# Performance work log

Hardware: AMD Instinct MI355X
Metric: run time of the kernel (lower is better)

## Reference

```python
import jax, jax.numpy as jnp
import numpy as np

B, S, IN_DIM = 8, 1024, 512
EMBED_DIM, NUM_HEADS = 512, 8
HEAD_DIM = EMBED_DIM // NUM_HEADS
LN_EPS = 1e-5


def setup_inputs() -> dict:
    key = jax.random.key(0)
    k1, k2, k3 = jax.random.split(key, 3)
    x = jax.random.normal(k1, (B, S, IN_DIM), dtype=jnp.float32)
    # xavier_uniform for qkv_proj.weight [3*embed, in] and o_proj.weight [embed, embed]
    lim_qkv = float(np.sqrt(6.0 / (3 * EMBED_DIM + IN_DIM)))
    w_qkv = jax.random.uniform(k2, (3 * EMBED_DIM, IN_DIM), dtype=jnp.float32,
                               minval=-lim_qkv, maxval=lim_qkv)
    lim_o = float(np.sqrt(6.0 / (EMBED_DIM + EMBED_DIM)))
    w_o = jax.random.uniform(k3, (EMBED_DIM, EMBED_DIM), dtype=jnp.float32,
                             minval=-lim_o, maxval=lim_o)
    return {"x": x, "w_qkv": w_qkv, "w_o": w_o}


def reference(x, w_qkv, w_o):
    b, s, _ = x.shape
    # fused QKV projection: [b, s, 3*embed]
    qkv = jnp.einsum('bsi,ei->bse', x, w_qkv)
    # [b, h, s, 3*head_dim]
    qkv = qkv.reshape(b, s, NUM_HEADS, 3 * HEAD_DIM).transpose(0, 2, 1, 3)
    q, k, v = jnp.split(qkv, 3, axis=-1)
    scale = 1.0 / np.sqrt(HEAD_DIM)
    logits = jnp.einsum('bhqd,bhkd->bhqk', q, k) * scale  # [b, h, s, s]
    attn = jax.nn.softmax(logits, axis=-1)
    vals = jnp.einsum('bhqk,bhkd->bhqd', attn, v)
    vals = vals.transpose(0, 2, 1, 3).reshape(b, s, EMBED_DIM)
    o = jnp.einsum('bse,fe->bsf', vals, w_o)
    # LayerNorm over [seq, embed] jointly (fresh nn.LayerNorm([N, D]): weight=1, bias=0)
    mu = jnp.mean(o, axis=(-2, -1), keepdims=True)
    var = jnp.var(o, axis=(-2, -1), keepdims=True)
    o = (o - mu) / jnp.sqrt(var + LN_EPS)
    return o
```

## Files before the change

### kernel.cpp

```cpp
#include <hip/hip_runtime.h>
#include <hip/hip_bf16.h>
#include <math.h>

#define BB 8
#define SS 1024
#define INDIM 512
#define ED 512
#define NH 8
#define HD 64

typedef __attribute__((ext_vector_type(8))) short short8;
typedef __attribute__((ext_vector_type(4))) float f32x4;
typedef __attribute__((ext_vector_type(16))) float f32x16;
typedef unsigned short u16;

typedef __attribute__((address_space(1))) const void gv_t;
typedef __attribute__((address_space(3))) void lv_t;

static __device__ __forceinline__ u16 f2bf(float f) {
  union { float f; unsigned u; } v; v.f = f;
  unsigned r = v.u + 0x7fffu + ((v.u >> 16) & 1u);
  return (u16)(r >> 16);
}
static __device__ __forceinline__ float bf2f(u16 b) {
  union { unsigned u; float f; } v; v.u = (unsigned)b << 16; return v.f;
}

static __device__ __forceinline__ unsigned cvt_pk_bf16(float a, float b) {
  unsigned r;
  asm("v_cvt_pk_bf16_f32 %0, %1, %2" : "=v"(r) : "v"(a), "v"(b));
  return r;
}
static __device__ __forceinline__ float fast_exp2(float x) {
  float r; asm("v_exp_f32 %0, %1" : "=v"(r) : "v"(x)); return r;
}

__global__ void cvt_all(const float* __restrict__ x, const float* __restrict__ wq,
                        const float* __restrict__ wo, u16* __restrict__ xb,
                        u16* __restrict__ wqb, u16* __restrict__ wob) {
  const int n1 = 1048576;
  const int n2 = n1 + 196608;
  const int n3 = n2 + 65536;
  int i = blockIdx.x * blockDim.x + threadIdx.x;
  int stride = gridDim.x * blockDim.x;
  for (; i < n3; i += stride) {
    const float4* src; ushort4* dst; int j;
    if (i < n1)      { src = (const float4*)x;  dst = (ushort4*)xb;  j = i; }
    else if (i < n2) { src = (const float4*)wq; dst = (ushort4*)wqb; j = i - n1; }
    else             { src = (const float4*)wo; dst = (ushort4*)wob; j = i - n2; }
    float4 v = src[j];
    ushort4 o;
    o.x = f2bf(v.x); o.y = f2bf(v.y); o.z = f2bf(v.z); o.w = f2bf(v.w);
    dst[j] = o;
  }
}

template<int EPI>
__global__ __launch_bounds__(256, 2)
void gemm_nt(const u16* __restrict__ A, const u16* __restrict__ Bm, int K,
             u16* __restrict__ outB,
             u16* __restrict__ qws, u16* __restrict__ kws, u16* __restrict__ vtws,
             float2* __restrict__ partials)
{
  __shared__ u16 As[128][64];
  __shared__ u16 Bs[128][64];
  const int tid = threadIdx.x;
  const int lane = tid & 63;
  const int wv = tid >> 6;
  const int wr = wv >> 1, wc = wv & 1;
  const int bm = blockIdx.x, bn = blockIdx.y;
  const int l15 = lane & 15, lg = lane >> 4;
  const int srow8 = lane >> 3;
  const int sc8 = lane & 7;

  f32x4 acc[4][4];
  #pragma unroll
  for (int i = 0; i < 4; i++)
    #pragma unroll
    for (int j = 0; j < 4; j++) acc[i][j] = (f32x4){0.f, 0.f, 0.f, 0.f};

  for (int kk = 0; kk < K; kk += 64) {
    #pragma unroll
    for (int i = 0; i < 4; i++) {
      int r0 = (i * 4 + wv) * 8;
      int r = r0 + srow8;
      int cs = sc8 ^ (r & 7);
      const u16* ga = A + (size_t)(bm * 128 + r) * K + kk + cs * 8;
      __builtin_amdgcn_global_load_lds((gv_t*)ga, (lv_t*)&As[r0][0], 16, 0, 0);
      const u16* gb = Bm + (size_t)(bn * 128 + r) * K + kk + cs * 8;
      __builtin_amdgcn_global_load_lds((gv_t*)gb, (lv_t*)&Bs[r0][0], 16, 0, 0);
    }
    __syncthreads();
    #pragma unroll
    for (int kc = 0; kc < 2; kc++) {
      short8 af[4], bf[4];
      #pragma unroll
      for (int mi = 0; mi < 4; mi++) {
        int ra = wr * 64 + mi * 16 + l15;
        af[mi] = *(const short8*)&As[ra][((kc * 4 + lg) ^ (ra & 7)) * 8];
      }
      #pragma unroll
      for (int ni = 0; ni < 4; ni++) {
        int rb = wc * 64 + ni * 16 + l15;
        bf[ni] = *(const short8*)&Bs[rb][((kc * 4 + lg) ^ (rb & 7)) * 8];
      }
      #pragma unroll
      for (int mi = 0; mi < 4; mi++)
        #pragma unroll
        for (int ni = 0; ni < 4; ni++)
          acc[mi][ni] = __builtin_amdgcn_mfma_f32_16x16x32_bf16(af[mi], bf[ni], acc[mi][ni], 0, 0, 0);
    }
    __syncthreads();
  }

  if constexpr (EPI == 0) {
    #pragma unroll
    for (int mi = 0; mi < 4; mi++) {
      int rowg = bm * 128 + wr * 64 + mi * 16 + lg * 4;
      #pragma unroll
      for (int ni = 0; ni < 4; ni++) {
        int colg = bn * 128 + wc * 64 + ni * 16 + l15;
        int h = colg / 192, c = colg - h * 192;
        #pragma unroll
        for (int r = 0; r < 4; r++) {
          int rg = rowg + r;
          float v = acc[mi][ni][r];
          int b = rg >> 10, s = rg & 1023;
          int bh = b * 8 + h;
          if (c < 64)
            qws[((size_t)(bh * 1024 + s)) * 64 + c] = f2bf(v * 0.18033688f);
          else if (c < 128)
            kws[((size_t)(bh * 1024 + s)) * 64 + (c - 64)] = f2bf(v);
        }
      }
    }
    const int rem = (bn * 128) % 192;
    if (rem != 0) {
      __shared__ u16 T[64][136];
      const int vbase = (rem == 128) ? 0 : 64;
      if (wc == (vbase >> 6)) {
        #pragma unroll
        for (int mi = 0; mi < 4; mi++) {
          int trow0 = wr * 64 + mi * 16 + lg * 4;
          #pragma unroll
          for (int ni = 0; ni < 4; ni++) {
            int tcol = ni * 16 + l15;
            u16 tmp[4];
            #pragma unroll
            for (int r = 0; r < 4; r++) tmp[r] = f2bf(acc[mi][ni][r]);
            *(uint2*)&T[tcol][trow0] = *(const uint2*)tmp;
          }
        }
      }
      __syncthreads();
      const int h = (bn * 128 + vbase) / 192;
      const int bh = (bm >> 3) * 8 + h;
      const int col = tid >> 2, q4 = tid & 3;
      u16* dst = vtws + ((size_t)(bh * 64 + col)) * 1024 + (bm & 7) * 128 + q4 * 32;
      const u16* src = &T[col][q4 * 32];
      #pragma unroll
      for (int k2 = 0; k2 < 4; k2++)
        *(uint4*)(dst + k2 * 8) = *(const uint4*)(src + k2 * 8);
    }
  } else {
    float s1 = 0.f, s2 = 0.f;
    #pragma unroll
    for (int mi = 0; mi < 4; mi++) {
      int rowg = bm * 128 + wr * 64 + mi * 16 + lg * 4;
      #pragma unroll
      for (int ni = 0; ni < 4; ni++) {
        int colg = bn * 128 + wc * 64 + ni * 16 + l15;
        #pragma unroll
        for (int r = 0; r < 4; r++) {
          float v = acc[mi][ni][r];
          s1 += v; s2 += v * v;
          outB[(size_t)(rowg + r) * 512 + colg] = f2bf(v);
        }
      }
    }
    #pragma unroll
    for (int off = 1; off < 64; off <<= 1) {
      s1 += __shfl_xor(s1, off);
      s2 += __shfl_xor(s2, off);
    }
    __shared__ float r1[4], r2[4];
    if (lane == 0) { r1[wv] = s1; r2[wv] = s2; }
    __syncthreads();
    if (tid == 0) {
      float t1 = r1[0] + r1[1] + r1[2] + r1[3];
      float t2 = r2[0] + r2[1] + r2[2] + r2[3];
      partials[bm * 4 + bn] = make_float2(t1, t2);
    }
  }
}

__global__ __launch_bounds__(512, 4)
void attn_kernel(const u16* __restrict__ qws, const u16* __restrict__ kws,
                 const u16* __restrict__ vtws, u16* __restrict__ vals)
{
  __shared__ __align__(16) u16 Ksm[2][64][72];
  __shared__ __align__(16) u16 Vsm[2][64][72];
  const int tid = threadIdx.x;
  const int lane = tid & 63;
  const int wq = tid >> 6;
  const int l31 = lane & 31;
  const int hi = lane >> 5;
  const int logical = (blockIdx.x & 7) * 32 + (blockIdx.x >> 3);
  const int bh = logical >> 2;
  const int q0 = (logical & 3) * 256;

  short8 qf[4];
  {
    const u16* qp = qws + ((size_t)bh * 1024 + q0 + wq * 32 + l31) * 64 + 8 * hi;
    #pragma unroll
    for (int j = 0; j < 4; j++) qf[j] = *(const short8*)(qp + 16 * j);
  }

  const int srow = tid >> 3;
  const int sc8 = (tid & 7) * 8;
  uint4 kreg, vreg;
  kreg = *(const uint4*)(kws + ((size_t)bh * 1024 + srow) * 64 + sc8);
  vreg = *(const uint4*)(vtws + ((size_t)(bh * 64 + srow)) * 1024 + sc8);
  *(uint4*)&Ksm[0][srow][sc8] = kreg;
  *(uint4*)&Vsm[0][srow][sc8] = vreg;
  __syncthreads();

  f32x16 o[2];
  #pragma unroll
  for (int r = 0; r < 16; r++) { o[0][r] = 0.f; o[1][r] = 0.f; }
  float m = -1e30f, l = 0.f;

  for (int t = 0; t < 16; t++) {
    const int cur = t & 1;
    if (t < 15) {
      int kv = (t + 1) * 64;
      kreg = *(const uint4*)(kws + ((size_t)bh * 1024 + kv + srow) * 64 + sc8);
      vreg = *(const uint4*)(vtws + ((size_t)(bh * 64 + srow)) * 1024 + kv + sc8);
    }

    f32x16 stv[2];
    __builtin_amdgcn_s_setprio(1);
    #pragma unroll
    for (int s2 = 0; s2 < 2; s2++) {
      f32x16 c;
      #pragma unroll
      for (int r = 0; r < 16; r++) c[r] = 0.f;
      #pragma unroll
      for (int j = 0; j < 4; j++) {
        short8 kf = *(const short8*)&Ksm[cur][s2 * 32 + l31][16 * j + 8 * hi];
        c = __builtin_amdgcn_mfma_f32_32x32x16_bf16(kf, qf[j], c, 0, 0, 0);
      }
      stv[s2] = c;
    }
    __builtin_amdgcn_s_setprio(0);

    float mx[16];
    #pragma unroll
    for (int r = 0; r < 16; r++) mx[r] = fmaxf(stv[0][r], stv[1][r]);
    #pragma unroll
    for (int w = 8; w >= 1; w >>= 1)
      #pragma unroll
      for (int r = 0; r < w; r++) mx[r] = fmaxf(mx[r], mx[r + w]);
    float pm = fmaxf(mx[0], __shfl_xor(mx[0], 32));

    if (!__all(pm - m <= 10.0f)) {
      float mn = fmaxf(m, pm);
      float al = fast_exp2(m - mn);
      m = mn; l *= al;
      #pragma unroll
      for (int reg = 0; reg < 16; reg++) {
        int qrow = (reg & 3) + 8 * (reg >> 2) + 4 * hi;
        float alo = __shfl(al, qrow);
        o[0][reg] *= alo; o[1][reg] *= alo;
      }
    }

    unsigned pk[16];
    float ps[16];
    #pragma unroll
    for (int s2 = 0; s2 < 2; s2++)
      #pragma unroll
      for (int j = 0; j < 8; j++) {
        float p0 = fast_exp2(stv[s2][2 * j] - m);
        float p1 = fast_exp2(stv[s2][2 * j + 1] - m);
        ps[s2 * 8 + j] = p0 + p1;
        pk[s2 * 8 + j] = cvt_pk_bf16(p0, p1);
      }
    #pragma unroll
    for (int w = 8; w >= 1; w >>= 1)
      #pragma unroll
      for (int r = 0; r < w; r++) ps[r] += ps[r + w];
    l += ps[0] + __shfl_xor(ps[0], 32);

    short8 pa[4];
    #pragma unroll
    for (int cc = 0; cc < 4; cc++) {
      int base = (cc >> 1) * 8 + (cc & 1) * 4;
      unsigned a0 = pk[base + 0], a2 = pk[base + 2];
      unsigned a1 = pk[base + 1], a3 = pk[base + 3];
      asm volatile("v_permlane32_swap_b32 %0, %1" : "+v"(a0), "+v"(a2));
      asm volatile("v_permlane32_swap_b32 %0, %1" : "+v"(a1), "+v"(a3));
      union { unsigned u[4]; short8 s8; } uu;
      uu.u[0] = a0; uu.u[1] = a1; uu.u[2] = a2; uu.u[3] = a3;
      pa[cc] = uu.s8;
    }

    __builtin_amdgcn_s_setprio(1);
    #pragma unroll
    for (int dh = 0; dh < 2; dh++)
      #pragma unroll
      for (int cc = 0; cc < 4; cc++) {
        short8 vf = *(const short8*)&Vsm[cur][dh * 32 + l31][16 * cc + 8 * hi];
        o[dh] = __builtin_amdgcn_mfma_f32_32x32x16_bf16(pa[cc], vf, o[dh], 0, 0, 0);
      }
    __builtin_amdgcn_s_setprio(0);

    if (t < 15) {
      *(uint4*)&Ksm[cur ^ 1][srow][sc8] = kreg;
      *(uint4*)&Vsm[cur ^ 1][srow][sc8] = vreg;
    }
    __syncthreads();
  }

  const int b = bh >> 3, h = bh & 7;
  #pragma unroll
  for (int reg = 0; reg < 16; reg++) {
    int qrow = (reg & 3) + 8 * (reg >> 2) + 4 * hi;
    float linv = 1.0f / __shfl(l, qrow);
    size_t grow = (size_t)(b * 1024 + q0 + wq * 32 + qrow) * 512 + h * 64;
    vals[grow + l31]      = f2bf(o[0][reg] * linv);
    vals[grow + 32 + l31] = f2bf(o[1][reg] * linv);
  }
}

__global__ void ln_norm3(const u16* __restrict__ ob, float* __restrict__ o,
                         const float2* __restrict__ partials) {
  const int blk = blockIdx.x;
  const int b = blk >> 8;
  const int lane = threadIdx.x & 63;
  float s1 = 0.f, s2 = 0.f;
  if (lane < 32) {
    float2 p = partials[b * 32 + lane];
    s1 = p.x; s2 = p.y;
  }
  #pragma unroll
  for (int off = 1; off < 64; off <<= 1) {
    s1 += __shfl_xor(s1, off);
    s2 += __shfl_xor(s2, off);
  }
  float mu = s1 / 524288.f;
  float rs = rsqrtf(s2 / 524288.f - mu * mu + 1e-5f);
  const size_t i = (size_t)blk * 2048 + threadIdx.x * 8;
  uint4 v = *(const uint4*)(ob + i);
  float4 o0, o1;
  o0.x = (bf2f((u16)(v.x & 0xffff)) - mu) * rs;
  o0.y = (bf2f((u16)(v.x >> 16)) - mu) * rs;
  o0.z = (bf2f((u16)(v.y & 0xffff)) - mu) * rs;
  o0.w = (bf2f((u16)(v.y >> 16)) - mu) * rs;
  o1.x = (bf2f((u16)(v.z & 0xffff)) - mu) * rs;
  o1.y = (bf2f((u16)(v.z >> 16)) - mu) * rs;
  o1.z = (bf2f((u16)(v.w & 0xffff)) - mu) * rs;
  o1.w = (bf2f((u16)(v.w >> 16)) - mu) * rs;
  *(float4*)(o + i) = o0;
  *(float4*)(o + i + 4) = o1;
}

extern "C" void kernel_launch(void* const* d_in, const int* in_sizes, int n_in,
                              void* d_out, int out_size, void* d_ws, size_t ws_size,
                              hipStream_t stream) {
  const float* x = (const float*)d_in[0];
  const float* wqkv = (const float*)d_in[1];
  const float* wo = (const float*)d_in[2];
  float* out = (float*)d_out;
  char* ws = (char*)d_ws;

  u16* xb        = (u16*)(ws + 0);
  u16* wqb       = (u16*)(ws + 8388608);
  u16* wob       = (u16*)(ws + 9961472);
  u16* qws       = (u16*)(ws + 10485760);
  u16* kws       = (u16*)(ws + 18874368);
  u16* vtws      = (u16*)(ws + 27262976);
  u16* vals      = (u16*)(ws + 35651584);
  u16* outb      = (u16*)(ws + 44040192);
  float2* parts  = (float2*)(ws + 52428800);

  cvt_all<<<1280, 256, 0, stream>>>(x, wqkv, wo, xb, wqb, wob);

  dim3 g1(64, 12);
  gemm_nt<0><<<g1, 256, 0, stream>>>(xb, wqb, 512, nullptr, qws, kws, vtws, nullptr);

  attn_kernel<<<256, 512, 0, stream>>>(qws, kws, vtws, vals);

  dim3 g2(64, 4);
  gemm_nt<1><<<g2, 256, 0, stream>>>(vals, wob, 512, outb, nullptr, nullptr, nullptr, parts);

  ln_norm3<<<2048, 256, 0, stream>>>(outb, out, parts);
}
```

Before: 76.37 us.

## Fuse output projection GEMM with LayerNorm via cooperative grid sync

Merges the output-projection GEMM and the LayerNorm normalisation into one cooperative kernel. Each block computes its partial sums, all blocks meet at a grid-wide sync, and each block then normalises its accumulators still in registers and writes fp32 output directly. This removes the bf16 intermediate write and read and one kernel launch. In exchange it adds the cost of a grid barrier and a cooperative launch, and it requires all 256 blocks to be resident at the same time.

```diff
diff --git a/kernel.cpp b/kernel.cpp
--- a/kernel.cpp
+++ b/kernel.cpp
@@ -1,6 +1,9 @@
 #include <hip/hip_runtime.h>
 #include <hip/hip_bf16.h>
+#include <hip/hip_cooperative_groups.h>
 #include <math.h>
+
+namespace cg = cooperative_groups;
 
 #define BB 8
 #define SS 1024
@@ -55,12 +58,9 @@
   }
 }
 
-template<int EPI>
 __global__ __launch_bounds__(256, 2)
-void gemm_nt(const u16* __restrict__ A, const u16* __restrict__ Bm, int K,
-             u16* __restrict__ outB,
-             u16* __restrict__ qws, u16* __restrict__ kws, u16* __restrict__ vtws,
-             float2* __restrict__ partials)
+void gemm_qkv(const u16* __restrict__ A, const u16* __restrict__ Bm, int K,
+              u16* __restrict__ qws, u16* __restrict__ kws, u16* __restrict__ vtws)
 {
   __shared__ u16 As[128][64];
   __shared__ u16 Bs[128][64];
@@ -113,83 +113,161 @@
     __syncthreads();
   }
 
-  if constexpr (EPI == 0) {
-    #pragma unroll
-    for (int mi = 0; mi < 4; mi++) {
-      int rowg = bm * 128 + wr * 64 + mi * 16 + lg * 4;
+  #pragma unroll
+  for (int mi = 0; mi < 4; mi++) {
+    int rowg = bm * 128 + wr * 64 + mi * 16 + lg * 4;
+    #pragma unroll
+    for (int ni = 0; ni < 4; ni++) {
+      int colg = bn * 128 + wc * 64 + ni * 16 + l15;
+      int h = colg / 192, c = colg - h * 192;
+      #pragma unroll
+      for (int r = 0; r < 4; r++) {
+        int rg = rowg + r;
+        float v = acc[mi][ni][r];
+        int b = rg >> 10, s = rg & 1023;
+        int bh = b * 8 + h;
+        if (c < 64)
+          qws[((size_t)(bh * 1024 + s)) * 64 + c] = f2bf(v * 0.18033688f);
+        else if (c < 128)
+          kws[((size_t)(bh * 1024 + s)) * 64 + (c - 64)] = f2bf(v);
+      }
+    }
+  }
+  const int rem = (bn * 128) % 192;
+  if (rem != 0) {
+    __shared__ u16 T[64][136];
+    const int vbase = (rem == 128) ? 0 : 64;
+    if (wc == (vbase >> 6)) {
+      #pragma unroll
+      for (int mi = 0; mi < 4; mi++) {
+        int trow0 = wr * 64 + mi * 16 + lg * 4;
+        #pragma unroll
+        for (int ni = 0; ni < 4; ni++) {
+          int tcol = ni * 16 + l15;
+          u16 tmp[4];
+          #pragma unroll
+          for (int r = 0; r < 4; r++) tmp[r] = f2bf(acc[mi][ni][r]);
+          *(uint2*)&T[tcol][trow0] = *(const uint2*)tmp;
+        }
+      }
+    }
+    __syncthreads();
+    const int h = (bn * 128 + vbase) / 192;
+    const int bh = (bm >> 3) * 8 + h;
+    const int col = tid >> 2, q4 = tid & 3;
+    u16* dst = vtws + ((size_t)(bh * 64 + col)) * 1024 + (bm & 7) * 128 + q4 * 32;
+    const u16* src = &T[col][q4 * 32];
+    #pragma unroll
+    for (int k2 = 0; k2 < 4; k2++)
+      *(uint4*)(dst + k2 * 8) = *(const uint4*)(src + k2 * 8);
+  }
+}
+
+__global__ __launch_bounds__(256, 2)
+void gemm_o_ln(const u16* __restrict__ A, const u16* __restrict__ Bm,
+               float* __restrict__ outF, float2* __restrict__ partials)
+{
+  __shared__ u16 As[128][64];
+  __shared__ u16 Bs[128][64];
+  const int K = 512;
+  const int tid = threadIdx.x;
+  const int lane = tid & 63;
+  const int wv = tid >> 6;
+  const int wr = wv >> 1, wc = wv & 1;
+  const int bm = blockIdx.x, bn = blockIdx.y;
+  const int l15 = lane & 15, lg = lane >> 4;
+  const int srow8 = lane >> 3;
+  const int sc8 = lane & 7;
+
+  f32x4 acc[4][4];
+  #pragma unroll
+  for (int i = 0; i < 4; i++)
+    #pragma unroll
+    for (int j = 0; j < 4; j++) acc[i][j] = (f32x4){0.f, 0.f, 0.f, 0.f};
+
+  for (int kk = 0; kk < K; kk += 64) {
+    #pragma unroll
+    for (int i = 0; i < 4; i++) {
+      int r0 = (i * 4 + wv) * 8;
+      int r = r0 + srow8;
+      int cs = sc8 ^ (r & 7);
+      const u16* ga = A + (size_t)(bm * 128 + r) * K + kk + cs * 8;
+      __builtin_amdgcn_global_load_lds((gv_t*)ga, (lv_t*)&As[r0][0], 16, 0, 0);
+      const u16* gb = Bm + (size_t)(bn * 128 + r) * K + kk + cs * 8;
+      __builtin_amdgcn_global_load_lds((gv_t*)gb, (lv_t*)&Bs[r0][0], 16, 0, 0);
+    }
+    __syncthreads();
+    #pragma unroll
+    for (int kc = 0; kc < 2; kc++) {
+      short8 af[4], bf[4];
+      #pragma unroll
+      for (int mi = 0; mi < 4; mi++) {
+        int ra = wr * 64 + mi * 16 + l15;
+        af[mi] = *(const short8*)&As[ra][((kc * 4 + lg) ^ (ra & 7)) * 8];
+      }
       #pragma unroll
       for (int ni = 0; ni < 4; ni++) {
-        int colg = bn * 128 + wc * 64 + ni * 16 + l15;
-        int h = colg / 192, c = colg - h * 192;
+        int rb = wc * 64 + ni * 16 + l15;
+        bf[ni] = *(const short8*)&Bs[rb][((kc * 4 + lg) ^ (rb & 7)) * 8];
+      }
+      #pragma unroll
+      for (int mi = 0; mi < 4; mi++)
         #pragma unroll
-        for (int r = 0; r < 4; r++) {
-          int rg = rowg + r;
-          float v = acc[mi][ni][r];
-          int b = rg >> 10, s = rg & 1023;
-          int bh = b * 8 + h;
-          if (c < 64)
-            qws[((size_t)(bh * 1024 + s)) * 64 + c] = f2bf(v * 0.18033688f);
-          else if (c < 128)
-            kws[((size_t)(bh * 1024 + s)) * 64 + (c - 64)] = f2bf(v);
-        }
-      }
-    }
-    const int rem = (bn * 128) % 192;
-    if (rem != 0) {
-      __shared__ u16 T[64][136];
-      const int vbase = (rem == 128) ? 0 : 64;
-      if (wc == (vbase >> 6)) {
-        #pragma unroll
-        for (int mi = 0; mi < 4; mi++) {
-          int trow0 = wr * 64 + mi * 16 + lg * 4;
-          #pragma unroll
-          for (int ni = 0; ni < 4; ni++) {
-            int tcol = ni * 16 + l15;
-            u16 tmp[4];
-            #pragma unroll
-            for (int r = 0; r < 4; r++) tmp[r] = f2bf(acc[mi][ni][r]);
-            *(uint2*)&T[tcol][trow0] = *(const uint2*)tmp;
-          }
-        }
-      }
-      __syncthreads();
-      const int h = (bn * 128 + vbase) / 192;
-      const int bh = (bm >> 3) * 8 + h;
-      const int col = tid >> 2, q4 = tid & 3;
-      u16* dst = vtws + ((size_t)(bh * 64 + col)) * 1024 + (bm & 7) * 128 + q4 * 32;
-      const u16* src = &T[col][q4 * 32];
-      #pragma unroll
-      for (int k2 = 0; k2 < 4; k2++)
-        *(uint4*)(dst + k2 * 8) = *(const uint4*)(src + k2 * 8);
-    }
-  } else {
-    float s1 = 0.f, s2 = 0.f;
-    #pragma unroll
-    for (int mi = 0; mi < 4; mi++) {
-      int rowg = bm * 128 + wr * 64 + mi * 16 + lg * 4;
-      #pragma unroll
-      for (int ni = 0; ni < 4; ni++) {
-        int colg = bn * 128 + wc * 64 + ni * 16 + l15;
-        #pragma unroll
-        for (int r = 0; r < 4; r++) {
-          float v = acc[mi][ni][r];
-          s1 += v; s2 += v * v;
-          outB[(size_t)(rowg + r) * 512 + colg] = f2bf(v);
-        }
-      }
-    }
-    #pragma unroll
-    for (int off = 1; off < 64; off <<= 1) {
-      s1 += __shfl_xor(s1, off);
-      s2 += __shfl_xor(s2, off);
-    }
-    __shared__ float r1[4], r2[4];
-    if (lane == 0) { r1[wv] = s1; r2[wv] = s2; }
-    __syncthreads();
-    if (tid == 0) {
-      float t1 = r1[0] + r1[1] + r1[2] + r1[3];
-      float t2 = r2[0] + r2[1] + r2[2] + r2[3];
-      partials[bm * 4 + bn] = make_float2(t1, t2);
+        for (int ni = 0; ni < 4; ni++)
+          acc[mi][ni] = __builtin_amdgcn_mfma_f32_16x16x32_bf16(af[mi], bf[ni], acc[mi][ni], 0, 0, 0);
+    }
+    __syncthreads();
+  }
+
+  float s1 = 0.f, s2 = 0.f;
+  #pragma unroll
+  for (int mi = 0; mi < 4; mi++)
+    #pragma unroll
+    for (int ni = 0; ni < 4; ni++)
+      #pragma unroll
+      for (int r = 0; r < 4; r++) {
+        float v = acc[mi][ni][r];
+        s1 += v; s2 += v * v;
+      }
+  #pragma unroll
+  for (int off = 1; off < 64; off <<= 1) {
+    s1 += __shfl_xor(s1, off);
+    s2 += __shfl_xor(s2, off);
+  }
+  __shared__ float r1[4], r2[4];
+  if (lane == 0) { r1[wv] = s1; r2[wv] = s2; }
+  __syncthreads();
+  if (tid == 0) {
+    float t1 = r1[0] + r1[1] + r1[2] + r1[3];
+    float t2 = r2[0] + r2[1] + r2[2] + r2[3];
+    partials[bm * 4 + bn] = make_float2(t1, t2);
+    __threadfence();
+  }
+
+  cg::this_grid().sync();
+
+  float a = 0.f, c = 0.f;
+  if (lane < 32) {
+    float2 p = partials[(bm >> 3) * 32 + lane];
+    a = p.x; c = p.y;
+  }
+  #pragma unroll
+  for (int off = 1; off < 64; off <<= 1) {
+    a += __shfl_xor(a, off);
+    c += __shfl_xor(c, off);
+  }
+  float mu = a / 524288.f;
+  float rs = rsqrtf(c / 524288.f - mu * mu + 1e-5f);
+
+  #pragma unroll
+  for (int mi = 0; mi < 4; mi++) {
+    int rowg = bm * 128 + wr * 64 + mi * 16 + lg * 4;
+    #pragma unroll
+    for (int ni = 0; ni < 4; ni++) {
+      int colg = bn * 128 + wc * 64 + ni * 16 + l15;
+      #pragma unroll
+      for (int r = 0; r < 4; r++)
+        outF[(size_t)(rowg + r) * 512 + colg] = (acc[mi][ni][r] - mu) * rs;
     }
   }
 }
@@ -333,38 +411,6 @@
   }
 }
 
-__global__ void ln_norm3(const u16* __restrict__ ob, float* __restrict__ o,
-                         const float2* __restrict__ partials) {
-  const int blk = blockIdx.x;
-  const int b = blk >> 8;
-  const int lane = threadIdx.x & 63;
-  float s1 = 0.f, s2 = 0.f;
-  if (lane < 32) {
-    float2 p = partials[b * 32 + lane];
-    s1 = p.x; s2 = p.y;
-  }
-  #pragma unroll
-  for (int off = 1; off < 64; off <<= 1) {
-    s1 += __shfl_xor(s1, off);
-    s2 += __shfl_xor(s2, off);
-  }
-  float mu = s1 / 524288.f;
-  float rs = rsqrtf(s2 / 524288.f - mu * mu + 1e-5f);
-  const size_t i = (size_t)blk * 2048 + threadIdx.x * 8;
-  uint4 v = *(const uint4*)(ob + i);
-  float4 o0, o1;
-  o0.x = (bf2f((u16)(v.x & 0xffff)) - mu) * rs;
-  o0.y = (bf2f((u16)(v.x >> 16)) - mu) * rs;
-  o0.z = (bf2f((u16)(v.y & 0xffff)) - mu) * rs;
-  o0.w = (bf2f((u16)(v.y >> 16)) - mu) * rs;
-  o1.x = (bf2f((u16)(v.z & 0xffff)) - mu) * rs;
-  o1.y = (bf2f((u16)(v.z >> 16)) - mu) * rs;
-  o1.z = (bf2f((u16)(v.w & 0xffff)) - mu) * rs;
-  o1.w = (bf2f((u16)(v.w >> 16)) - mu) * rs;
-  *(float4*)(o + i) = o0;
-  *(float4*)(o + i + 4) = o1;
-}
-
 extern "C" void kernel_launch(void* const* d_in, const int* in_sizes, int n_in,
                               void* d_out, int out_size, void* d_ws, size_t ws_size,
                               hipStream_t stream) {
@@ -381,18 +427,22 @@
   u16* kws       = (u16*)(ws + 18874368);
   u16* vtws      = (u16*)(ws + 27262976);
   u16* vals      = (u16*)(ws + 35651584);
-  u16* outb      = (u16*)(ws + 44040192);
-  float2* parts  = (float2*)(ws + 52428800);
+  float2* parts  = (float2*)(ws + 44040192);
 
   cvt_all<<<1280, 256, 0, stream>>>(x, wqkv, wo, xb, wqb, wob);
 
   dim3 g1(64, 12);
-  gemm_nt<0><<<g1, 256, 0, stream>>>(xb, wqb, 512, nullptr, qws, kws, vtws, nullptr);
+  gemm_qkv<<<g1, 256, 0, stream>>>(xb, wqb, 512, qws, kws, vtws);
 
   attn_kernel<<<256, 512, 0, stream>>>(qws, kws, vtws, vals);
 
-  dim3 g2(64, 4);
-  gemm_nt<1><<<g2, 256, 0, stream>>>(vals, wob, 512, outb, nullptr, nullptr, nullptr, parts);
-
-  ln_norm3<<<2048, 256, 0, stream>>>(outb, out, parts);
-}
+  {
+    const u16* a = vals;
+    const u16* b = wob;
+    float* o = out;
+    float2* p = parts;
+    void* args[] = {(void*)&a, (void*)&b, (void*)&o, (void*)&p};
+    hipLaunchCooperativeKernel((void*)gemm_o_ln, dim3(64, 4), dim3(256),
+                               args, 0, stream);
+  }
+}
```

New measurement: 127.3 us. +66.7%, slower.
